# Performance work log

Measured on AMD Instinct MI355X. Metric: run time of the kernel, lower is better.

Reference implementation:

```python
import jax, jax.numpy as jnp
import numpy as np

EMBED = 1024
HEADS = 16
HEAD_DIM = EMBED // HEADS


def setup_inputs() -> dict:
    key = jax.random.key(0)
    ks = jax.random.split(key, 9)
    s = 1.0 / np.sqrt(EMBED)
    x = jax.random.normal(ks[0], (2, 2048, EMBED), dtype=jnp.float32)
    Wq = jax.random.uniform(ks[1], (EMBED, EMBED), jnp.float32, -s, s)
    bq = jax.random.uniform(ks[2], (EMBED,), jnp.float32, -s, s)
    Wk = jax.random.uniform(ks[3], (EMBED, EMBED), jnp.float32, -s, s)
    bk = jax.random.uniform(ks[4], (EMBED,), jnp.float32, -s, s)
    Wv = jax.random.uniform(ks[5], (EMBED, EMBED), jnp.float32, -s, s)
    bv = jax.random.uniform(ks[6], (EMBED,), jnp.float32, -s, s)
    Wo = jax.random.uniform(ks[7], (EMBED, EMBED), jnp.float32, -s, s)
    bo = jax.random.uniform(ks[8], (EMBED,), jnp.float32, -s, s)
    return {"x": x, "Wq": Wq, "bq": bq, "Wk": Wk, "bk": bk,
            "Wv": Wv, "bv": bv, "Wo": Wo, "bo": bo}


def reference(x, Wq, bq, Wk, bk, Wv, bv, Wo, bo):
    B, S, E = x.shape
    H, D = HEADS, HEAD_DIM
    # QKV projections, split heads: [B,S,E] -> [B,H,S,D]
    def proj(W, b):
        return (x @ W + b).reshape(B, S, H, D).transpose(0, 2, 1, 3)
    q, k, v = proj(Wq, bq), proj(Wk, bk), proj(Wv, bv)
    scores = jnp.einsum('bhsd,bhtd->bhst', q, k) / jnp.sqrt(jnp.float32(D))
    attn = jax.nn.softmax(scores, axis=-1)
    out = jnp.einsum('bhst,bhtd->bhsd', attn, v)  # [B,H,S,D]
    out = out.transpose(0, 2, 1, 3).reshape(B, S, E)
    return out @ Wo + bo
```

## Files before the change

kernel.cpp:

```cpp
#include <hip/hip_runtime.h>
#include <cstddef>
#include <cstdint>

#define EMB 1024
#define NH 16
#define HD 64
#define SEQ 2048
#define BATCH 2
#define MROWS 4096
#define LOG2E 1.4426950408889634f

typedef unsigned short u16;
typedef __attribute__((ext_vector_type(8))) short short8;
typedef __attribute__((ext_vector_type(4))) float floatx4;
typedef __attribute__((ext_vector_type(16))) float floatx16;

#define MFMA32(a,b,c) __builtin_amdgcn_mfma_f32_16x16x32_bf16((a),(b),(c),0,0,0)
#define MFMA3216(a,b,c) __builtin_amdgcn_mfma_f32_32x32x16_bf16((a),(b),(c),0,0,0)

__device__ __forceinline__ u16 f2bf(float f) {
    union { float f; uint32_t u; } v; v.f = f;
    return (u16)((v.u + 0x7fffu + ((v.u >> 16) & 1u)) >> 16);
}
__device__ __forceinline__ uint32_t pk2u(uint32_t a, uint32_t b) {
    return __builtin_amdgcn_perm(b, a, 0x07060302u);
}
__device__ __forceinline__ float lo_f(uint32_t u) {
    union { uint32_t u; float f; } v; v.u = u << 16; return v.f;
}
__device__ __forceinline__ float hi_f(uint32_t u) {
    union { uint32_t u; float f; } v; v.u = u & 0xffff0000u; return v.f;
}
__device__ __forceinline__ float trunc_bf(uint32_t u) {
    union { uint32_t u; float f; } v; v.u = u & 0xffff0000u; return v.f;
}
__device__ __forceinline__ uint32_t exp2_fast_bits(float s) {
    return (uint32_t)(int)fmaf(s, 8388608.0f, 1064992512.0f);
}
__device__ __forceinline__ void plswap(uint32_t &a, uint32_t &b) {
    asm volatile("v_permlane32_swap_b32 %0, %1" : "+v"(a), "+v"(b));
}
typedef const __attribute__((address_space(1))) void* gptr_t;
typedef __attribute__((address_space(3))) void* lptr_t;
__device__ __forceinline__ void gl2lds16(const void* g, void* l) {
    __builtin_amdgcn_global_load_lds((gptr_t)g, (lptr_t)l, 16, 0, 0);
}

__global__ __launch_bounds__(256) void cvt_all_k(
    const float* __restrict__ x,
    const float* __restrict__ W0, const float* __restrict__ W1,
    const float* __restrict__ W2, const float* __restrict__ W3,
    u16* __restrict__ Wt4, u16* __restrict__ xh) {
    const int z = blockIdx.z;
    const int tid = threadIdx.x;
    if (z == 4) {
        const int nb = gridDim.x * gridDim.y;
        const int bid = blockIdx.y * gridDim.x + blockIdx.x;
        const int stride = nb * 256 * 8;
        for (int i = (bid * 256 + tid) * 8; i < MROWS * EMB; i += stride) {
            float4 a = *(const float4*)(x + i);
            float4 b = *(const float4*)(x + i + 4);
            alignas(16) u16 o[8] = {f2bf(a.x), f2bf(a.y), f2bf(a.z), f2bf(a.w),
                                    f2bf(b.x), f2bf(b.y), f2bf(b.z), f2bf(b.w)};
            *(uint4*)(xh + i) = *(const uint4*)o;
        }
        return;
    }
    const float* W = (z == 0) ? W0 : (z == 1) ? W1 : (z == 2) ? W2 : W3;
    const float scale = (z == 0) ? 0.125f * LOG2E : 1.0f;
    u16* dst = Wt4 + (size_t)z * 1048576;
    __shared__ float Lf[64][65];
    const int kt = blockIdx.y * 64, nt = blockIdx.x * 64;
    {
        const int r = tid >> 2, c4 = (tid & 3) * 16;
        const float* src = W + (size_t)(kt + r) * EMB + nt + c4;
        #pragma unroll
        for (int i = 0; i < 16; i += 4) {
            float4 v = *(const float4*)(src + i);
            Lf[r][c4 + i + 0] = v.x; Lf[r][c4 + i + 1] = v.y;
            Lf[r][c4 + i + 2] = v.z; Lf[r][c4 + i + 3] = v.w;
        }
    }
    __syncthreads();
    const int n = tid >> 2, k4 = (tid & 3) * 16;
    alignas(16) u16 hb[16];
    #pragma unroll
    for (int i = 0; i < 16; ++i) hb[i] = f2bf(Lf[k4 + i][n] * scale);
    const size_t o = (size_t)(nt + n) * EMB + kt + k4;
    *(uint4*)(dst + o) = *(const uint4*)hb;
    *(uint4*)(dst + o + 8) = *(const uint4*)(hb + 8);
}

__global__ __launch_bounds__(256) void gemm_qkv_k(
    const u16* __restrict__ xh, const u16* __restrict__ Wt4,
    const float* __restrict__ b0, const float* __restrict__ b1,
    const float* __restrict__ b2,
    u16* __restrict__ Q, u16* __restrict__ K, u16* __restrict__ V) {
    const int z = blockIdx.z;
    const u16* Wt = Wt4 + (size_t)z * 1048576;
    const float* bias = (z == 0) ? b0 : (z == 1) ? b1 : b2;
    u16* out = (z == 0) ? Q : (z == 1) ? K : V;
    const float bscale = (z == 0) ? 0.125f * LOG2E : 1.0f;
    const int bm = blockIdx.y * 128, bn = blockIdx.x * 128;
    __shared__ alignas(16) u16 As[4096];
    __shared__ alignas(16) u16 Bs[4096];
    const int tid = threadIdx.x;
    const int lane = tid & 63, w = tid >> 6;
    const int l15 = lane & 15, quad = lane >> 4;
    const int wm = (w & 1) * 64, wn = (w >> 1) * 64;

    floatx4 acc[4][4];
    const floatx4 zf = {0.f, 0.f, 0.f, 0.f};
    #pragma unroll
    for (int mt = 0; mt < 4; ++mt)
        #pragma unroll
        for (int nt = 0; nt < 4; ++nt) acc[mt][nt] = zf;

    const int c0 = tid, c1 = tid + 256;
    const int r0 = c0 >> 2, p0 = c0 & 3, cc0 = (p0 - r0 - (r0 >> 2)) & 3;
    const int r1 = c1 >> 2, p1 = c1 & 3, cc1 = (p1 - r1 - (r1 >> 2)) & 3;
    const u16* ag0 = xh + (size_t)(bm + r0) * EMB + cc0 * 8;
    const u16* ag1 = xh + (size_t)(bm + r1) * EMB + cc1 * 8;
    const u16* bg0 = Wt + (size_t)(bn + r0) * EMB + cc0 * 8;
    const u16* bg1 = Wt + (size_t)(bn + r1) * EMB + cc1 * 8;

    for (int kt = 0; kt < EMB; kt += 32) {
        __syncthreads();
        gl2lds16(ag0 + kt, &As[c0 * 8]); gl2lds16(ag1 + kt, &As[c1 * 8]);
        gl2lds16(bg0 + kt, &Bs[c0 * 8]); gl2lds16(bg1 + kt, &Bs[c1 * 8]);
        __syncthreads();
        short8 af[4], bf[4];
        #pragma unroll
        for (int t = 0; t < 4; ++t) {
            const int ra = wm + t * 16 + l15;
            const int rb = wn + t * 16 + l15;
            af[t] = *(const short8*)&As[ra * 32 + ((quad + ra + (ra >> 2)) & 3) * 8];
            bf[t] = *(const short8*)&Bs[rb * 32 + ((quad + rb + (rb >> 2)) & 3) * 8];
        }
        #pragma unroll
        for (int mt = 0; mt < 4; ++mt)
            #pragma unroll
            for (int nt = 0; nt < 4; ++nt)
                acc[mt][nt] = MFMA32(af[mt], bf[nt], acc[mt][nt]);
    }

    #pragma unroll
    for (int nt = 0; nt < 4; ++nt) {
        const int col = bn + wn + nt * 16 + l15;
        const float bv = bias[col] * bscale;
        #pragma unroll
        for (int mt = 0; mt < 4; ++mt) {
            const int row = bm + wm + mt * 16 + quad * 4;
            #pragma unroll
            for (int r = 0; r < 4; ++r)
                out[(size_t)(row + r) * EMB + col] = f2bf(acc[mt][nt][r] + bv);
        }
    }
}

__global__ __launch_bounds__(256) void gemm_o_k(
    const u16* __restrict__ Ag, const u16* __restrict__ Wt,
    const float* __restrict__ bias, float* __restrict__ out) {
    const int bm = blockIdx.y * 128, bn = blockIdx.x * 64;
    __shared__ alignas(16) u16 As[4096];
    __shared__ alignas(16) u16 Bs[2048];
    const int tid = threadIdx.x;
    const int lane = tid & 63, w = tid >> 6;
    const int l15 = lane & 15, quad = lane >> 4;
    const int wm = w * 32;

    floatx4 acc[2][4];
    const floatx4 zf = {0.f, 0.f, 0.f, 0.f};
    #pragma unroll
    for (int mt = 0; mt < 2; ++mt)
        #pragma unroll
        for (int nt = 0; nt < 4; ++nt) acc[mt][nt] = zf;

    const int c0 = tid, c1 = tid + 256;
    const int r0 = c0 >> 2, p0 = c0 & 3, cc0 = (p0 - r0 - (r0 >> 2)) & 3;
    const int r1 = c1 >> 2, p1 = c1 & 3, cc1 = (p1 - r1 - (r1 >> 2)) & 3;
    const u16* ag0 = Ag + (size_t)(bm + r0) * EMB + cc0 * 8;
    const u16* ag1 = Ag + (size_t)(bm + r1) * EMB + cc1 * 8;
    const u16* bg0 = Wt + (size_t)(bn + r0) * EMB + cc0 * 8;

    for (int kt = 0; kt < EMB; kt += 32) {
        __syncthreads();
        gl2lds16(ag0 + kt, &As[c0 * 8]);
        gl2lds16(ag1 + kt, &As[c1 * 8]);
        if (c0 < 256) gl2lds16(bg0 + kt, &Bs[c0 * 8]);
        __syncthreads();
        short8 af[2], bf[4];
        #pragma unroll
        for (int t = 0; t < 2; ++t) {
            const int ra = wm + t * 16 + l15;
            af[t] = *(const short8*)&As[ra * 32 + ((quad + ra + (ra >> 2)) & 3) * 8];
        }
        #pragma unroll
        for (int t = 0; t < 4; ++t) {
            const int rb = t * 16 + l15;
            bf[t] = *(const short8*)&Bs[rb * 32 + ((quad + rb + (rb >> 2)) & 3) * 8];
        }
        #pragma unroll
        for (int mt = 0; mt < 2; ++mt)
            #pragma unroll
            for (int nt = 0; nt < 4; ++nt)
                acc[mt][nt] = MFMA32(af[mt], bf[nt], acc[mt][nt]);
    }

    #pragma unroll
    for (int nt = 0; nt < 4; ++nt) {
        const int col = bn + nt * 16 + l15;
        const float bv = bias[col];
        #pragma unroll
        for (int mt = 0; mt < 2; ++mt) {
            const int row = bm + wm + mt * 16 + quad * 4;
            #pragma unroll
            for (int r = 0; r < 4; ++r)
                out[(size_t)(row + r) * EMB + col] = acc[mt][nt][r] + bv;
        }
    }
}

__global__ __launch_bounds__(256) void vtrans_k(const u16* __restrict__ V,
                                                u16* __restrict__ Vt) {
    const int tt = blockIdx.x, h = blockIdx.y, b = blockIdx.z;
    __shared__ u16 Lt[64][72];
    const int tid = threadIdx.x;
    {
        const int r = tid >> 2, c4 = (tid & 3) * 16;
        const u16* src = V + (size_t)(b * SEQ + tt * 64 + r) * EMB + h * HD + c4;
        alignas(16) u16 buf[16];
        *(uint4*)buf = *(const uint4*)src;
        *(uint4*)(buf + 8) = *(const uint4*)(src + 8);
        #pragma unroll
        for (int i = 0; i < 16; ++i) Lt[c4 + i][r] = buf[i];
    }
    __syncthreads();
    const int d = tid >> 2, t4 = (tid & 3) * 16;
    u16* dst = Vt + ((size_t)((b * NH + h) * HD + d)) * SEQ + tt * 64 + t4;
    *(uint4*)dst = *(const uint4*)&Lt[d][t4];
    *(uint4*)(dst + 8) = *(const uint4*)&Lt[d][t4 + 8];
}

__global__ __launch_bounds__(256) void flash_k(
    const u16* __restrict__ Q, const u16* __restrict__ K,
    const u16* __restrict__ Vt,
    u16* __restrict__ Np0, u16* __restrict__ Np1,
    u16* __restrict__ Np2, u16* __restrict__ Np3,
    float* __restrict__ Lp) {
    const int qt = blockIdx.x, h = blockIdx.y;
    const int b = blockIdx.z >> 2, sp = blockIdx.z & 3;
    const int t0 = sp * (SEQ / 4);
    __shared__ alignas(16) u16 Ks[4096];
    __shared__ alignas(16) u16 Vs[4096];
    const int tid = threadIdx.x;
    const int lane = tid & 63, w = tid >> 6;
    const int l31 = lane & 31, hf = lane >> 5;

    const u16* qp = Q + (size_t)(b * SEQ + qt * 128 + w * 32 + l31) * EMB
                    + h * HD + hf * 8;
    short8 qb[4];
    #pragma unroll
    for (int c = 0; c < 4; ++c) qb[c] = *(const short8*)(qp + c * 16);

    const floatx16 z16 = {0.f, 0.f, 0.f, 0.f, 0.f, 0.f, 0.f, 0.f,
                          0.f, 0.f, 0.f, 0.f, 0.f, 0.f, 0.f, 0.f};
    floatx16 oacc[2];
    oacc[0] = z16; oacc[1] = z16;
    float lsum = 0.f;

    const int s0 = tid, s1 = tid + 256;
    const int kr0 = s0 >> 3, kc0 = ((s0 & 7) - kr0) & 7;
    const int kr1 = s1 >> 3, kc1 = ((s1 & 7) - kr1) & 7;
    const u16* kg0 = K + (size_t)(b * SEQ + t0 + kr0) * EMB + h * HD + kc0 * 8;
    const u16* kg1 = K + (size_t)(b * SEQ + t0 + kr1) * EMB + h * HD + kc1 * 8;
    const u16* vg0 = Vt + ((size_t)((b * NH + h) * HD + kr0)) * SEQ + t0 + kc0 * 8;
    const u16* vg1 = Vt + ((size_t)((b * NH + h) * HD + kr1)) * SEQ + t0 + kc1 * 8;

    for (int kt = 0; kt < SEQ / 4 / 64; ++kt) {
        __syncthreads();
        gl2lds16(kg0 + (size_t)kt * 64 * EMB, &Ks[s0 * 8]);
        gl2lds16(kg1 + (size_t)kt * 64 * EMB, &Ks[s1 * 8]);
        gl2lds16(vg0 + kt * 64, &Vs[s0 * 8]);
        gl2lds16(vg1 + kt * 64, &Vs[s1 * 8]);
        __syncthreads();

        short8 pa[4];
        #pragma unroll
        for (int tt = 0; tt < 2; ++tt) {
            floatx16 st = z16;
            const int r = tt * 32 + l31;
            #pragma unroll
            for (int c = 0; c < 4; ++c) {
                const int jc = c * 2 + hf;
                const short8 ka = *(const short8*)&Ks[r * 64 + ((jc + r) & 7) * 8];
                st = MFMA3216(ka, qb[c], st);
            }
            uint32_t e[16];
            #pragma unroll
            for (int i = 0; i < 16; ++i) e[i] = exp2_fast_bits(st[i]);
            #pragma unroll
            for (int i = 0; i < 16; ++i) lsum += trunc_bf(e[i]);
            #pragma unroll
            for (int c = 0; c < 2; ++c) {
                uint32_t w0 = pk2u(e[c * 8 + 0], e[c * 8 + 1]);
                uint32_t w1 = pk2u(e[c * 8 + 2], e[c * 8 + 3]);
                uint32_t w2 = pk2u(e[c * 8 + 4], e[c * 8 + 5]);
                uint32_t w3 = pk2u(e[c * 8 + 6], e[c * 8 + 7]);
                plswap(w0, w2);
                plswap(w1, w3);
                union { uint32_t uu[4]; short8 s; } pk_;
                pk_.uu[0] = w0; pk_.uu[1] = w1; pk_.uu[2] = w2; pk_.uu[3] = w3;
                pa[tt * 2 + c] = pk_.s;
            }
        }

        #pragma unroll
        for (int dt = 0; dt < 2; ++dt) {
            const int vr = dt * 32 + l31;
            #pragma unroll
            for (int g = 0; g < 4; ++g) {
                const int jc = g * 2 + hf;
                const short8 vb = *(const short8*)&Vs[vr * 64 + ((jc + vr) & 7) * 8];
                oacc[dt] = MFMA3216(pa[g], vb, oacc[dt]);
            }
        }
    }

    u16* np = (sp == 0) ? Np0 : (sp == 1) ? Np1 : (sp == 2) ? Np2 : Np3;
    float* lp = Lp + (size_t)sp * (MROWS * NH);

    lsum += __shfl_xor(lsum, 32);
    if (lane < 32) {
        const int qrow = qt * 128 + w * 32 + l31;
        lp[(size_t)(b * SEQ + qrow) * NH + h] = lsum;
    }

    #pragma unroll
    for (int dt = 0; dt < 2; ++dt)
        #pragma unroll
        for (int r = 0; r < 16; ++r) {
            const int qloc = (r & 3) + 8 * (r >> 2) + 4 * hf;
            const size_t o =
                (size_t)(b * SEQ + qt * 128 + w * 32 + qloc) * EMB
                + h * HD + dt * 32 + l31;
            np[o] = f2bf(oacc[dt][r]);
        }
}

__global__ __launch_bounds__(256) void reduce_k(
    const u16* __restrict__ Np0, const u16* __restrict__ Np1,
    const u16* __restrict__ Np2, const u16* __restrict__ Np3,
    const float* __restrict__ Lp, u16* __restrict__ AO) {
    const int i = blockIdx.x * 256 + threadIdx.x;
    const int e = i * 4;
    const int row = e >> 10;
    const int hh = (e & 1023) >> 6;
    const size_t lx = (size_t)row * NH + hh;
    const float lsum = Lp[lx] + Lp[(size_t)(MROWS * NH) + lx] +
                       Lp[2 * (size_t)(MROWS * NH) + lx] +
                       Lp[3 * (size_t)(MROWS * NH) + lx];
    const float inv = 1.f / lsum;
    const uint2 n0 = *(const uint2*)(Np0 + e);
    const uint2 n1 = *(const uint2*)(Np1 + e);
    const uint2 n2 = *(const uint2*)(Np2 + e);
    const uint2 n3 = *(const uint2*)(Np3 + e);
    const float x0 = (lo_f(n0.x) + lo_f(n1.x) + lo_f(n2.x) + lo_f(n3.x)) * inv;
    const float x1 = (hi_f(n0.x) + hi_f(n1.x) + hi_f(n2.x) + hi_f(n3.x)) * inv;
    const float x2 = (lo_f(n0.y) + lo_f(n1.y) + lo_f(n2.y) + lo_f(n3.y)) * inv;
    const float x3 = (hi_f(n0.y) + hi_f(n1.y) + hi_f(n2.y) + hi_f(n3.y)) * inv;
    uint2 o;
    o.x = (uint32_t)f2bf(x0) | ((uint32_t)f2bf(x1) << 16);
    o.y = (uint32_t)f2bf(x2) | ((uint32_t)f2bf(x3) << 16);
    *(uint2*)(AO + e) = o;
}

extern "C" void kernel_launch(void* const* d_in, const int* in_sizes, int n_in,
                              void* d_out, int out_size, void* d_ws, size_t ws_size,
                              hipStream_t stream) {
    const float* x  = (const float*)d_in[0];
    const float* Wq = (const float*)d_in[1];
    const float* bq = (const float*)d_in[2];
    const float* Wk = (const float*)d_in[3];
    const float* bk = (const float*)d_in[4];
    const float* Wv = (const float*)d_in[5];
    const float* bv = (const float*)d_in[6];
    const float* Wo = (const float*)d_in[7];
    const float* bo = (const float*)d_in[8];

    u16* ws16 = (u16*)d_ws;
    const size_t P4 = (size_t)MROWS * EMB;
    u16* xh  = ws16;
    u16* Qb  = ws16 + P4;
    u16* Kb  = ws16 + 2 * P4;
    u16* Vb  = ws16 + 3 * P4;
    u16* Vtb = ws16 + 4 * P4;
    u16* Wt4 = ws16 + 5 * P4;
    u16* N2  = ws16 + 6 * P4;
    u16* N3  = ws16 + 7 * P4;
    float* Lp = (float*)(ws16 + 8 * P4);

    cvt_all_k<<<dim3(16, 16, 5), 256, 0, stream>>>(x, Wq, Wk, Wv, Wo, Wt4, xh);
    gemm_qkv_k<<<dim3(8, 32, 3), 256, 0, stream>>>(xh, Wt4, bq, bk, bv, Qb, Kb, Vb);
    vtrans_k<<<dim3(32, 16, 2), 256, 0, stream>>>(Vb, Vtb);
    flash_k<<<dim3(16, 16, 8), 256, 0, stream>>>(Qb, Kb, Vtb, xh, Vb, N2, N3, Lp);
    reduce_k<<<4096, 256, 0, stream>>>(xh, Vb, N2, N3, Lp, Qb);
    gemm_o_k<<<dim3(16, 32, 1), 256, 0, stream>>>(Qb, Wt4 + 3 * 1048576, bo, (float*)d_out);
}
```

Baseline: 205.9 us.

## Double-buffer LDS tiles in GEMMs and attention, compute row sums via MFMA

```diff
diff --git a/kernel.cpp b/kernel.cpp
--- a/kernel.cpp
+++ b/kernel.cpp
@@ -14,6 +14,7 @@
 typedef __attribute__((ext_vector_type(8))) short short8;
 typedef __attribute__((ext_vector_type(4))) float floatx4;
 typedef __attribute__((ext_vector_type(16))) float floatx16;
+typedef __attribute__((ext_vector_type(2))) float f32x2;
 
 #define MFMA32(a,b,c) __builtin_amdgcn_mfma_f32_16x16x32_bf16((a),(b),(c),0,0,0)
 #define MFMA3216(a,b,c) __builtin_amdgcn_mfma_f32_32x32x16_bf16((a),(b),(c),0,0,0)
@@ -30,12 +31,6 @@
 }
 __device__ __forceinline__ float hi_f(uint32_t u) {
     union { uint32_t u; float f; } v; v.u = u & 0xffff0000u; return v.f;
-}
-__device__ __forceinline__ float trunc_bf(uint32_t u) {
-    union { uint32_t u; float f; } v; v.u = u & 0xffff0000u; return v.f;
-}
-__device__ __forceinline__ uint32_t exp2_fast_bits(float s) {
-    return (uint32_t)(int)fmaf(s, 8388608.0f, 1064992512.0f);
 }
 __device__ __forceinline__ void plswap(uint32_t &a, uint32_t &b) {
     asm volatile("v_permlane32_swap_b32 %0, %1" : "+v"(a), "+v"(b));
@@ -102,8 +97,8 @@
     u16* out = (z == 0) ? Q : (z == 1) ? K : V;
     const float bscale = (z == 0) ? 0.125f * LOG2E : 1.0f;
     const int bm = blockIdx.y * 128, bn = blockIdx.x * 128;
-    __shared__ alignas(16) u16 As[4096];
-    __shared__ alignas(16) u16 Bs[4096];
+    __shared__ alignas(16) u16 As[2][4096];
+    __shared__ alignas(16) u16 Bs[2][4096];
     const int tid = threadIdx.x;
     const int lane = tid & 63, w = tid >> 6;
     const int l15 = lane & 15, quad = lane >> 4;
@@ -124,24 +119,31 @@
     const u16* bg0 = Wt + (size_t)(bn + r0) * EMB + cc0 * 8;
     const u16* bg1 = Wt + (size_t)(bn + r1) * EMB + cc1 * 8;
 
+    #define QSTAGE(bf, kk) do { \
+        gl2lds16(ag0 + (kk), &As[bf][c0 * 8]); gl2lds16(ag1 + (kk), &As[bf][c1 * 8]); \
+        gl2lds16(bg0 + (kk), &Bs[bf][c0 * 8]); gl2lds16(bg1 + (kk), &Bs[bf][c1 * 8]); } while (0)
+
+    QSTAGE(0, 0);
+    __syncthreads();
     for (int kt = 0; kt < EMB; kt += 32) {
-        __syncthreads();
-        gl2lds16(ag0 + kt, &As[c0 * 8]); gl2lds16(ag1 + kt, &As[c1 * 8]);
-        gl2lds16(bg0 + kt, &Bs[c0 * 8]); gl2lds16(bg1 + kt, &Bs[c1 * 8]);
-        __syncthreads();
+        const int cur = (kt >> 5) & 1;
+        if (kt + 32 < EMB) QSTAGE(cur ^ 1, kt + 32);
         short8 af[4], bf[4];
         #pragma unroll
         for (int t = 0; t < 4; ++t) {
             const int ra = wm + t * 16 + l15;
             const int rb = wn + t * 16 + l15;
-            af[t] = *(const short8*)&As[ra * 32 + ((quad + ra + (ra >> 2)) & 3) * 8];
-            bf[t] = *(const short8*)&Bs[rb * 32 + ((quad + rb + (rb >> 2)) & 3) * 8];
-        }
+            af[t] = *(const short8*)&As[cur][ra * 32 + ((quad + ra + (ra >> 2)) & 3) * 8];
+            bf[t] = *(const short8*)&Bs[cur][rb * 32 + ((quad + rb + (rb >> 2)) & 3) * 8];
+        }
+        __builtin_amdgcn_s_setprio(1);
         #pragma unroll
         for (int mt = 0; mt < 4; ++mt)
             #pragma unroll
             for (int nt = 0; nt < 4; ++nt)
                 acc[mt][nt] = MFMA32(af[mt], bf[nt], acc[mt][nt]);
+        __builtin_amdgcn_s_setprio(0);
+        __syncthreads();
     }
 
     #pragma unroll
@@ -162,8 +164,8 @@
     const u16* __restrict__ Ag, const u16* __restrict__ Wt,
     const float* __restrict__ bias, float* __restrict__ out) {
     const int bm = blockIdx.y * 128, bn = blockIdx.x * 64;
-    __shared__ alignas(16) u16 As[4096];
-    __shared__ alignas(16) u16 Bs[2048];
+    __shared__ alignas(16) u16 As[2][4096];
+    __shared__ alignas(16) u16 Bs[2][2048];
     const int tid = threadIdx.x;
     const int lane = tid & 63, w = tid >> 6;
     const int l15 = lane & 15, quad = lane >> 4;
@@ -183,28 +185,35 @@
     const u16* ag1 = Ag + (size_t)(bm + r1) * EMB + cc1 * 8;
     const u16* bg0 = Wt + (size_t)(bn + r0) * EMB + cc0 * 8;
 
+    #define OSTAGE(bf, kk) do { \
+        gl2lds16(ag0 + (kk), &As[bf][c0 * 8]); \
+        gl2lds16(ag1 + (kk), &As[bf][c1 * 8]); \
+        if (c0 < 256) gl2lds16(bg0 + (kk), &Bs[bf][c0 * 8]); } while (0)
+
+    OSTAGE(0, 0);
+    __syncthreads();
     for (int kt = 0; kt < EMB; kt += 32) {
-        __syncthreads();
-        gl2lds16(ag0 + kt, &As[c0 * 8]);
-        gl2lds16(ag1 + kt, &As[c1 * 8]);
-        if (c0 < 256) gl2lds16(bg0 + kt, &Bs[c0 * 8]);
-        __syncthreads();
+        const int cur = (kt >> 5) & 1;
+        if (kt + 32 < EMB) OSTAGE(cur ^ 1, kt + 32);
         short8 af[2], bf[4];
         #pragma unroll
         for (int t = 0; t < 2; ++t) {
             const int ra = wm + t * 16 + l15;
-            af[t] = *(const short8*)&As[ra * 32 + ((quad + ra + (ra >> 2)) & 3) * 8];
+            af[t] = *(const short8*)&As[cur][ra * 32 + ((quad + ra + (ra >> 2)) & 3) * 8];
         }
         #pragma unroll
         for (int t = 0; t < 4; ++t) {
             const int rb = t * 16 + l15;
-            bf[t] = *(const short8*)&Bs[rb * 32 + ((quad + rb + (rb >> 2)) & 3) * 8];
-        }
+            bf[t] = *(const short8*)&Bs[cur][rb * 32 + ((quad + rb + (rb >> 2)) & 3) * 8];
+        }
+        __builtin_amdgcn_s_setprio(1);
         #pragma unroll
         for (int mt = 0; mt < 2; ++mt)
             #pragma unroll
             for (int nt = 0; nt < 4; ++nt)
                 acc[mt][nt] = MFMA32(af[mt], bf[nt], acc[mt][nt]);
+        __builtin_amdgcn_s_setprio(0);
+        __syncthreads();
     }
 
     #pragma unroll
@@ -251,8 +260,8 @@
     const int qt = blockIdx.x, h = blockIdx.y;
     const int b = blockIdx.z >> 2, sp = blockIdx.z & 3;
     const int t0 = sp * (SEQ / 4);
-    __shared__ alignas(16) u16 Ks[4096];
-    __shared__ alignas(16) u16 Vs[4096];
+    __shared__ alignas(16) u16 Ks[2][4096];
+    __shared__ alignas(16) u16 Vs[2][4096];
     const int tid = threadIdx.x;
     const int lane = tid & 63, w = tid >> 6;
     const int l31 = lane & 31, hf = lane >> 5;
@@ -267,7 +276,9 @@
                           0.f, 0.f, 0.f, 0.f, 0.f, 0.f, 0.f, 0.f};
     floatx16 oacc[2];
     oacc[0] = z16; oacc[1] = z16;
-    float lsum = 0.f;
+    floatx16 lacc = z16;
+    const short8 ones8 = {0x3F80, 0x3F80, 0x3F80, 0x3F80,
+                          0x3F80, 0x3F80, 0x3F80, 0x3F80};
 
     const int s0 = tid, s1 = tid + 256;
     const int kr0 = s0 >> 3, kc0 = ((s0 & 7) - kr0) & 7;
@@ -277,30 +288,40 @@
     const u16* vg0 = Vt + ((size_t)((b * NH + h) * HD + kr0)) * SEQ + t0 + kc0 * 8;
     const u16* vg1 = Vt + ((size_t)((b * NH + h) * HD + kr1)) * SEQ + t0 + kc1 * 8;
 
-    for (int kt = 0; kt < SEQ / 4 / 64; ++kt) {
-        __syncthreads();
-        gl2lds16(kg0 + (size_t)kt * 64 * EMB, &Ks[s0 * 8]);
-        gl2lds16(kg1 + (size_t)kt * 64 * EMB, &Ks[s1 * 8]);
-        gl2lds16(vg0 + kt * 64, &Vs[s0 * 8]);
-        gl2lds16(vg1 + kt * 64, &Vs[s1 * 8]);
-        __syncthreads();
+    #define FSTAGE(bf, kk) do { \
+        gl2lds16(kg0 + (size_t)(kk) * 64 * EMB, &Ks[bf][s0 * 8]); \
+        gl2lds16(kg1 + (size_t)(kk) * 64 * EMB, &Ks[bf][s1 * 8]); \
+        gl2lds16(vg0 + (kk) * 64, &Vs[bf][s0 * 8]); \
+        gl2lds16(vg1 + (kk) * 64, &Vs[bf][s1 * 8]); } while (0)
+
+    const int NT = SEQ / 4 / 64;
+    FSTAGE(0, 0);
+    __syncthreads();
+    for (int kt = 0; kt < NT; ++kt) {
+        const int cur = kt & 1;
+        if (kt + 1 < NT) FSTAGE(cur ^ 1, kt + 1);
 
         short8 pa[4];
         #pragma unroll
         for (int tt = 0; tt < 2; ++tt) {
             floatx16 st = z16;
             const int r = tt * 32 + l31;
+            __builtin_amdgcn_s_setprio(1);
             #pragma unroll
             for (int c = 0; c < 4; ++c) {
                 const int jc = c * 2 + hf;
-                const short8 ka = *(const short8*)&Ks[r * 64 + ((jc + r) & 7) * 8];
+                const short8 ka = *(const short8*)&Ks[cur][r * 64 + ((jc + r) & 7) * 8];
                 st = MFMA3216(ka, qb[c], st);
             }
+            __builtin_amdgcn_s_setprio(0);
             uint32_t e[16];
             #pragma unroll
-            for (int i = 0; i < 16; ++i) e[i] = exp2_fast_bits(st[i]);
-            #pragma unroll
-            for (int i = 0; i < 16; ++i) lsum += trunc_bf(e[i]);
+            for (int i = 0; i < 16; i += 2) {
+                f32x2 v = {st[i], st[i + 1]};
+                v = v * 8388608.0f + 1064992512.0f;
+                e[i] = (uint32_t)(int)v.x;
+                e[i + 1] = (uint32_t)(int)v.y;
+            }
             #pragma unroll
             for (int c = 0; c < 2; ++c) {
                 uint32_t w0 = pk2u(e[c * 8 + 0], e[c * 8 + 1]);
@@ -315,25 +336,34 @@
             }
         }
 
+        __builtin_amdgcn_s_setprio(1);
         #pragma unroll
         for (int dt = 0; dt < 2; ++dt) {
             const int vr = dt * 32 + l31;
             #pragma unroll
             for (int g = 0; g < 4; ++g) {
                 const int jc = g * 2 + hf;
-                const short8 vb = *(const short8*)&Vs[vr * 64 + ((jc + vr) & 7) * 8];
+                const short8 vb = *(const short8*)&Vs[cur][vr * 64 + ((jc + vr) & 7) * 8];
                 oacc[dt] = MFMA3216(pa[g], vb, oacc[dt]);
             }
         }
+        #pragma unroll
+        for (int g = 0; g < 4; ++g) lacc = MFMA3216(pa[g], ones8, lacc);
+        __builtin_amdgcn_s_setprio(0);
+
+        __syncthreads();
     }
 
     u16* np = (sp == 0) ? Np0 : (sp == 1) ? Np1 : (sp == 2) ? Np2 : Np3;
     float* lp = Lp + (size_t)sp * (MROWS * NH);
 
-    lsum += __shfl_xor(lsum, 32);
-    if (lane < 32) {
-        const int qrow = qt * 128 + w * 32 + l31;
-        lp[(size_t)(b * SEQ + qrow) * NH + h] = lsum;
+    if (l31 == 0) {
+        #pragma unroll
+        for (int r = 0; r < 16; ++r) {
+            const int qloc = (r & 3) + 8 * (r >> 2) + 4 * hf;
+            const int qrow = qt * 128 + w * 32 + qloc;
+            lp[(size_t)(b * SEQ + qrow) * NH + h] = lacc[r];
+        }
     }
 
     #pragma unroll
```

Measured after the change: 205.5 us. No clear change (-0.2%).
